# Performance work log

Measured on AMD Instinct MI355X. Metric: run time of the kernel, lower is better.

Reference implementation:

```python
import jax, jax.numpy as jnp
import numpy as np
import math

EMBED_DIM = 1024
NUM_HEADS = 16
HEAD_DIM = EMBED_DIM // NUM_HEADS


def setup_inputs() -> dict:
    key = jax.random.key(0)
    ks = jax.random.split(key, 5)
    s = 1.0 / math.sqrt(EMBED_DIM)
    return {
        "x": jax.random.normal(ks[0], (2, 2048, EMBED_DIM), dtype=jnp.float32),
        "w_qkv": jax.random.normal(ks[1], (EMBED_DIM, 3 * EMBED_DIM), dtype=jnp.float32) * s,
        "b_qkv": jax.random.normal(ks[2], (3 * EMBED_DIM,), dtype=jnp.float32) * 0.01,
        "w_proj": jax.random.normal(ks[3], (EMBED_DIM, EMBED_DIM), dtype=jnp.float32) * s,
        "b_proj": jax.random.normal(ks[4], (EMBED_DIM,), dtype=jnp.float32) * 0.01,
    }


def reference(x, w_qkv, b_qkv, w_proj, b_proj):
    B, T, C = x.shape
    qkv = (x @ w_qkv + b_qkv).reshape(B, T, 3, NUM_HEADS, HEAD_DIM)
    q, k, v = qkv[:, :, 0], qkv[:, :, 1], qkv[:, :, 2]  # [B,T,H,D]
    # scores: [B,H,T,T]
    att = jnp.einsum("bqhd,bkhd->bhqk", q, k) / math.sqrt(HEAD_DIM)
    causal = jnp.tril(jnp.ones((T, T), dtype=bool))
    att = jnp.where(causal[None, None], att, -jnp.inf)
    att = jax.nn.softmax(att, axis=-1)
    out = jnp.einsum("bhqk,bkhd->bqhd", att, v).reshape(B, T, C)
    return out @ w_proj + b_proj
```

## Files before the change

kernel.cpp:

```cpp
#include <hip/hip_runtime.h>
#include <stdint.h>


#define B_  2
#define T_  2048
#define C_  1024
#define NH  16
#define HD  64
#define BH_ (B_*NH)
#define M_  (B_*T_)

typedef __attribute__((ext_vector_type(8))) short short8;
typedef __attribute__((ext_vector_type(4))) float f32x4;
typedef __attribute__((ext_vector_type(4))) uint32_t u32x4;

typedef const __attribute__((address_space(1))) void* gas_ptr;
typedef __attribute__((address_space(3))) void* las_ptr;

__device__ __forceinline__ void gload_lds16(const void* g, void* l) {
  __builtin_amdgcn_global_load_lds((gas_ptr)g, (las_ptr)l, 16, 0, 0);
}

__device__ __forceinline__ unsigned short rne16(float x){
  uint32_t v = __float_as_uint(x);
  return (unsigned short)((v + 0x7fffu + ((v >> 16) & 1u)) >> 16);
}

__device__ __forceinline__ uint32_t cvtpk_bf16(float a, float b){
  uint32_t r;
  asm("v_cvt_pk_bf16_f32 %0, %1, %2" : "=v"(r) : "v"(a), "v"(b));
  return r;
}

__device__ __forceinline__ short8 hi8(u32x4 a, u32x4 b){
  union { u32x4 u; short8 s; } H;
  H.u[0] = __builtin_amdgcn_perm(a[1], a[0], 0x07060302u);
  H.u[1] = __builtin_amdgcn_perm(a[3], a[2], 0x07060302u);
  H.u[2] = __builtin_amdgcn_perm(b[1], b[0], 0x07060302u);
  H.u[3] = __builtin_amdgcn_perm(b[3], b[2], 0x07060302u);
  return H.s;
}
__device__ __forceinline__ short8 lo8(u32x4 a, u32x4 b){
  float l0 = __uint_as_float(a[0]) - __uint_as_float(a[0] & 0xffff0000u);
  float l1 = __uint_as_float(a[1]) - __uint_as_float(a[1] & 0xffff0000u);
  float l2 = __uint_as_float(a[2]) - __uint_as_float(a[2] & 0xffff0000u);
  float l3 = __uint_as_float(a[3]) - __uint_as_float(a[3] & 0xffff0000u);
  float l4 = __uint_as_float(b[0]) - __uint_as_float(b[0] & 0xffff0000u);
  float l5 = __uint_as_float(b[1]) - __uint_as_float(b[1] & 0xffff0000u);
  float l6 = __uint_as_float(b[2]) - __uint_as_float(b[2] & 0xffff0000u);
  float l7 = __uint_as_float(b[3]) - __uint_as_float(b[3] & 0xffff0000u);
  union { u32x4 u; short8 s; } L;
  L.u[0] = cvtpk_bf16(l0, l1);
  L.u[1] = cvtpk_bf16(l2, l3);
  L.u[2] = cvtpk_bf16(l4, l5);
  L.u[3] = cvtpk_bf16(l6, l7);
  return L.s;
}

__device__ __forceinline__ f32x4 mfma16(short8 a, short8 b, f32x4 c) {
  return __builtin_amdgcn_mfma_f32_16x16x32_bf16(a, b, c, 0, 0, 0);
}


__global__ __launch_bounds__(256) void pack4_kernel(const float4* __restrict__ in,
                                                    unsigned short* __restrict__ oh,
                                                    unsigned short* __restrict__ ol, int n4) {
  int i = blockIdx.x * 256 + threadIdx.x;
  if (i < n4) {
    float4 v = in[i];
    float f[4] = {v.x, v.y, v.z, v.w};
    ushort4 h, lo;
    unsigned short hh[4], ll[4];
    #pragma unroll
    for (int j=0;j<4;++j){
      uint32_t bt = __float_as_uint(f[j]);
      hh[j] = (unsigned short)(bt >> 16);
      ll[j] = rne16(f[j] - __uint_as_float(bt & 0xffff0000u));
    }
    h.x=hh[0]; h.y=hh[1]; h.z=hh[2]; h.w=hh[3];
    lo.x=ll[0]; lo.y=ll[1]; lo.z=ll[2]; lo.w=ll[3];
    *(ushort4*)(oh + (size_t)i*4) = h;
    *(ushort4*)(ol + (size_t)i*4) = lo;
  }
}

__global__ __launch_bounds__(1024) void pack_t_kernel(const float* __restrict__ in,
                                                      unsigned short* __restrict__ oh,
                                                      unsigned short* __restrict__ ol,
                                                      int R, int C) {
  __shared__ float tile[64][65];
  int c0 = blockIdx.x * 64, r0 = blockIdx.y * 64;
  int tx = threadIdx.x, ty = threadIdx.y;
  #pragma unroll
  for (int i = 0; i < 4; ++i)
    tile[ty + 16*i][tx] = in[(size_t)(r0 + ty + 16*i)*C + c0 + tx];
  __syncthreads();
  #pragma unroll
  for (int i = 0; i < 4; ++i) {
    float v = tile[tx][ty + 16*i];
    uint32_t bt = __float_as_uint(v);
    size_t o = (size_t)(c0 + ty + 16*i)*R + r0 + tx;
    oh[o] = (unsigned short)(bt >> 16);
    ol[o] = rne16(v - __uint_as_float(bt & 0xffff0000u));
  }
}


template<int MODE>
__global__ __launch_bounds__(256) void gemm_planes(
    const unsigned short* __restrict__ Ah, const unsigned short* __restrict__ Al,
    const unsigned short* __restrict__ Bh, const unsigned short* __restrict__ Bl,
    const float* __restrict__ bias,
    unsigned short* __restrict__ qh, unsigned short* __restrict__ ql,
    unsigned short* __restrict__ kh, unsigned short* __restrict__ kl,
    unsigned short* __restrict__ vth, unsigned short* __restrict__ vtl,
    float* __restrict__ fout, int M, int N, int K) {
  __shared__ unsigned short As[128*64];
  __shared__ unsigned short Bs[128*64];
  int tid = threadIdx.x;
  int w = tid >> 6, l = tid & 63, lg = l >> 4, lr = l & 15, lr7 = lr & 7;
  int bm = blockIdx.y * 128, bn = blockIdx.x * 128;
  int wm = (w >> 1) * 64, wn = (w & 1) * 64;

  const unsigned short* asrc[4]; const unsigned short* bsrc[4];
  #pragma unroll
  for (int i = 0; i < 4; ++i) {
    int s = tid + 256*i; int r = s >> 3, p = s & 7, u = p ^ (r & 7);
    asrc[i] = ((u < 4) ? Ah : Al) + (size_t)(bm + r)*K + (u & 3)*8;
    bsrc[i] = ((u < 4) ? Bh : Bl) + (size_t)(bn + r)*K + (u & 3)*8;
  }
  int aoh[4], boh[4];
  #pragma unroll
  for (int f = 0; f < 4; ++f) {
    aoh[f] = (wm + f*16 + lr)*128 + ((lg ^ lr7)*16);
    boh[f] = (wn + f*16 + lr)*128 + ((lg ^ lr7)*16);
  }

  f32x4 zero = {0.f, 0.f, 0.f, 0.f};
  f32x4 acc[4][4];
  #pragma unroll
  for (int i = 0; i < 4; ++i)
    #pragma unroll
    for (int j = 0; j < 4; ++j) acc[i][j] = zero;

  for (int k0 = 0; k0 < K; k0 += 32) {
    #pragma unroll
    for (int i = 0; i < 4; ++i) {
      int s = tid + 256*i;
      gload_lds16(asrc[i], (char*)As + (size_t)s*16);
      gload_lds16(bsrc[i], (char*)Bs + (size_t)s*16);
      asrc[i] += 32; bsrc[i] += 32;
    }
    __syncthreads();
    short8 ahf[4], alf[4];
    #pragma unroll
    for (int mf = 0; mf < 4; ++mf) {
      ahf[mf] = *(const short8*)((const char*)As + aoh[mf]);
      alf[mf] = *(const short8*)((const char*)As + (aoh[mf] ^ 64));
    }
    #pragma unroll
    for (int nf = 0; nf < 4; ++nf) {
      short8 bhf = *(const short8*)((const char*)Bs + boh[nf]);
      short8 blf = *(const short8*)((const char*)Bs + (boh[nf] ^ 64));
      #pragma unroll
      for (int mf = 0; mf < 4; ++mf) {
        acc[mf][nf] = mfma16(ahf[mf], bhf, acc[mf][nf]);
        acc[mf][nf] = mfma16(ahf[mf], blf, acc[mf][nf]);
        acc[mf][nf] = mfma16(alf[mf], bhf, acc[mf][nf]);
      }
    }
    __syncthreads();
  }
  #pragma unroll
  for (int nf = 0; nf < 4; ++nf) {
    int col = bn + wn + nf*16 + lr;
    float bv = bias[col];
    #pragma unroll
    for (int mf = 0; mf < 4; ++mf) {
      #pragma unroll
      for (int r = 0; r < 4; ++r) {
        int rowm = bm + wm + mf*16 + lg*4 + r;
        float v = acc[mf][nf][r] + bv;
        if (MODE == 1) {
          fout[(size_t)rowm*N + col] = v;
        } else {
          int sec = col >> 10;
          int hh  = (col >> 6) & 15;
          int d   = col & 63;
          int b   = rowm >> 11, t = rowm & 2047;
          size_t bhh = (size_t)b*NH + hh;
          if (sec == 0) v *= 0.125f;
          uint32_t bt = __float_as_uint(v);
          unsigned short h16 = (unsigned short)(bt >> 16);
          unsigned short l16 = rne16(v - __uint_as_float(bt & 0xffff0000u));
          if (sec == 0)      { size_t o = (bhh*T_ + t)*HD + d;  qh[o] = h16;  ql[o] = l16; }
          else if (sec == 1) { size_t o = (bhh*T_ + t)*HD + d;  kh[o] = h16;  kl[o] = l16; }
          else               { size_t o = (bhh*HD + d)*T_ + t;  vth[o] = h16; vtl[o] = l16; }
        }
      }
    }
  }
}


__global__ __launch_bounds__(256) void attn_kernel(
    const unsigned short* __restrict__ qh, const unsigned short* __restrict__ ql,
    const unsigned short* __restrict__ kh, const unsigned short* __restrict__ kl,
    const unsigned short* __restrict__ vth, const unsigned short* __restrict__ vtl,
    unsigned short* __restrict__ ctxh, unsigned short* __restrict__ ctxl) {
  __shared__ unsigned short Kt[2][64*128];
  __shared__ unsigned short Vt[2][64*128];
  __shared__ float Pf[4][1024];
  int bx = blockIdx.x;
  int xcd = bx & 7, jj = bx >> 3;
  int bh = xcd*4 + (jj >> 5);
  int qt = 31 - (jj & 31);
  int tid = threadIdx.x;
  int w = tid >> 6, l = tid & 63, lg = l >> 4, lr = l & 15, lr7 = lr & 7;
  int q0 = qt * 64;

  const unsigned short* qbh = qh + ((size_t)bh*T_ + q0 + w*16 + lr)*HD;
  const unsigned short* qbl = ql + ((size_t)bh*T_ + q0 + w*16 + lr)*HD;
  short8 qfh[2], qfl[2];
  #pragma unroll
  for (int ks = 0; ks < 2; ++ks) {
    qfh[ks] = *(const short8*)(qbh + ks*32 + lg*8);
    qfl[ks] = *(const short8*)(qbl + ks*32 + lg*8);
  }

  const unsigned short* ksrc[4]; const unsigned short* vsrc[4];
  #pragma unroll
  for (int i = 0; i < 4; ++i) {
    int s = tid + 256*i; int r = s >> 4, p = s & 15;
    int u = (p & 8) | ((p & 7) ^ (r & 7));
    ksrc[i] = ((u < 8) ? kh : kl) + ((size_t)bh*T_ + r)*HD + (u & 7)*8;
    vsrc[i] = ((u < 8) ? vth : vtl) + ((size_t)bh*HD + r)*T_ + (u & 7)*8;
  }
  auto stage = [&](int buf) {
    #pragma unroll
    for (int i = 0; i < 4; ++i) {
      int s = tid + 256*i;
      gload_lds16(ksrc[i], (char*)&Kt[buf][0] + (size_t)s*16);
      gload_lds16(vsrc[i], (char*)&Vt[buf][0] + (size_t)s*16);
    }
    #pragma unroll
    for (int i = 0; i < 4; ++i) { ksrc[i] += 64*HD; vsrc[i] += 64; }
  };

  int koff[4][2];
  #pragma unroll
  for (int fc = 0; fc < 4; ++fc)
    #pragma unroll
    for (int ks = 0; ks < 2; ++ks)
      koff[fc][ks] = (fc*16 + lr)*256 + (((ks*4 + lg) ^ lr7)*16);
  int pwoff[16];
  #pragma unroll
  for (int fc = 0; fc < 4; ++fc)
    #pragma unroll
    for (int r = 0; r < 4; ++r) {
      int q = lg*4 + r;
      int u = fc*4 + (lr >> 2);
      pwoff[fc*4 + r] = q*256 + ((u ^ q)*16) + (lr & 3)*4;
    }
  int proff[2][2];
  #pragma unroll
  for (int ks = 0; ks < 2; ++ks)
    #pragma unroll
    for (int g = 0; g < 2; ++g)
      proff[ks][g] = lr*256 + (((ks*8 + lg*2 + g) ^ lr)*16);

  f32x4 zero = {0.f, 0.f, 0.f, 0.f};
  f32x4 o[4] = {zero, zero, zero, zero};
  float m_r[4] = {-1e30f, -1e30f, -1e30f, -1e30f};
  float l_r[4] = {0.f, 0.f, 0.f, 0.f};
  char* PW = (char*)&Pf[w][0];

  stage(0);
  __syncthreads();
  int cur = 0;

  for (int kt = 0; kt <= qt; ++kt) {
    if (kt < qt) stage(cur ^ 1);
    const char* KB = (const char*)&Kt[cur][0];
    const char* VB = (const char*)&Vt[cur][0];
    f32x4 s4[4];
    #pragma unroll
    for (int fc = 0; fc < 4; ++fc) {
      f32x4 acc = zero;
      #pragma unroll
      for (int ks = 0; ks < 2; ++ks) {
        short8 khf = *(const short8*)(KB + koff[fc][ks]);
        short8 klf = *(const short8*)(KB + koff[fc][ks] + 128);
        acc = mfma16(qfh[ks], khf, acc);
        acc = mfma16(qfh[ks], klf, acc);
        acc = mfma16(qfl[ks], khf, acc);
      }
      s4[fc] = acc;
    }
    if (kt == qt) {
      #pragma unroll
      for (int fc = 0; fc < 4; ++fc)
        #pragma unroll
        for (int r = 0; r < 4; ++r) {
          int col = q0 + fc*16 + lr;
          int rw  = q0 + w*16 + lg*4 + r;
          if (col > rw) s4[fc][r] = -1e30f;
        }
    }
    float sc[4];
    #pragma unroll
    for (int r = 0; r < 4; ++r) {
      float v = fmaxf(fmaxf(s4[0][r], s4[1][r]), fmaxf(s4[2][r], s4[3][r]));
      v = fmaxf(v, __shfl_xor(v, 1));
      v = fmaxf(v, __shfl_xor(v, 2));
      v = fmaxf(v, __shfl_xor(v, 4));
      v = fmaxf(v, __shfl_xor(v, 8));
      float mn = fmaxf(m_r[r], v);
      sc[r] = __expf(m_r[r] - mn);
      m_r[r] = mn;
    }
    float sum[4] = {0.f, 0.f, 0.f, 0.f};
    #pragma unroll
    for (int fc = 0; fc < 4; ++fc)
      #pragma unroll
      for (int r = 0; r < 4; ++r) {
        float p = __expf(s4[fc][r] - m_r[r]);
        s4[fc][r] = p;
        sum[r] += p;
      }
    #pragma unroll
    for (int r = 0; r < 4; ++r) {
      float v = sum[r];
      v += __shfl_xor(v, 1); v += __shfl_xor(v, 2);
      v += __shfl_xor(v, 4); v += __shfl_xor(v, 8);
      l_r[r] = l_r[r]*sc[r] + v;
    }
    #pragma unroll
    for (int df = 0; df < 4; ++df)
      #pragma unroll
      for (int r = 0; r < 4; ++r) o[df][r] *= sc[r];
    #pragma unroll
    for (int fc = 0; fc < 4; ++fc)
      #pragma unroll
      for (int r = 0; r < 4; ++r)
        *(float*)(PW + pwoff[fc*4 + r]) = s4[fc][r];
    __builtin_amdgcn_sched_barrier(0);
    short8 pah[2], pal[2];
    #pragma unroll
    for (int ks = 0; ks < 2; ++ks) {
      u32x4 a = *(const u32x4*)(PW + proff[ks][0]);
      u32x4 b = *(const u32x4*)(PW + proff[ks][1]);
      pah[ks] = hi8(a, b);
      pal[ks] = lo8(a, b);
    }
    #pragma unroll
    for (int df = 0; df < 4; ++df) {
      #pragma unroll
      for (int ks = 0; ks < 2; ++ks) {
        short8 vhf = *(const short8*)(VB + koff[df][ks]);
        short8 vlf = *(const short8*)(VB + koff[df][ks] + 128);
        o[df] = mfma16(pah[ks], vhf, o[df]);
        o[df] = mfma16(pah[ks], vlf, o[df]);
        o[df] = mfma16(pal[ks], vhf, o[df]);
      }
    }
    __syncthreads();
    cur ^= 1;
  }
  int b = bh >> 4, h = bh & 15;
  float inv[4];
  #pragma unroll
  for (int r = 0; r < 4; ++r) inv[r] = 1.0f / l_r[r];
  #pragma unroll
  for (int df = 0; df < 4; ++df)
    #pragma unroll
    for (int r = 0; r < 4; ++r) {
      int q = q0 + w*16 + lg*4 + r;
      float v = o[df][r] * inv[r];
      uint32_t bt = __float_as_uint(v);
      size_t oo = ((size_t)b*T_ + q)*C_ + h*HD + df*16 + lr;
      ctxh[oo] = (unsigned short)(bt >> 16);
      ctxl[oo] = rne16(v - __uint_as_float(bt & 0xffff0000u));
    }
}


extern "C" void kernel_launch(void* const* d_in, const int* in_sizes, int n_in,
                              void* d_out, int out_size, void* d_ws, size_t ws_size,
                              hipStream_t stream) {
  (void)in_sizes; (void)n_in; (void)out_size; (void)ws_size;
  const float* x      = (const float*)d_in[0];
  const float* w_qkv  = (const float*)d_in[1];
  const float* b_qkv  = (const float*)d_in[2];
  const float* w_proj = (const float*)d_in[3];
  const float* b_proj = (const float*)d_in[4];
  float* out = (float*)d_out;

  uint8_t* ws = (uint8_t*)d_ws;
  const size_t MB = (size_t)1 << 20;
  unsigned short* xh  = (unsigned short*)(ws + 0);
  unsigned short* xl  = (unsigned short*)(ws + 8*MB);
  unsigned short* cth = xh;
  unsigned short* ctl = xl;
  unsigned short* wqh = (unsigned short*)(ws + 16*MB);
  unsigned short* wql = (unsigned short*)(ws + 22*MB);
  unsigned short* wph = (unsigned short*)(ws + 28*MB);
  unsigned short* wpl = (unsigned short*)(ws + 30*MB);
  unsigned short* qhp = (unsigned short*)(ws + 32*MB);
  unsigned short* qlp = (unsigned short*)(ws + 40*MB);
  unsigned short* khp = (unsigned short*)(ws + 48*MB);
  unsigned short* klp = (unsigned short*)(ws + 56*MB);
  unsigned short* vth = (unsigned short*)(ws + 64*MB);
  unsigned short* vtl = (unsigned short*)(ws + 72*MB);

  pack4_kernel<<<(M_*C_/4 + 255)/256, 256, 0, stream>>>((const float4*)x, xh, xl, M_*C_/4);
  pack_t_kernel<<<dim3(3*C_/64, C_/64), dim3(64, 16), 0, stream>>>(w_qkv, wqh, wql, C_, 3*C_);
  pack_t_kernel<<<dim3(C_/64, C_/64), dim3(64, 16), 0, stream>>>(w_proj, wph, wpl, C_, C_);
  gemm_planes<0><<<dim3(3*C_/128, M_/128), 256, 0, stream>>>(
      xh, xl, wqh, wql, b_qkv, qhp, qlp, khp, klp, vth, vtl, nullptr, M_, 3*C_, C_);
  attn_kernel<<<dim3(1024), 256, 0, stream>>>(qhp, qlp, khp, klp, vth, vtl, cth, ctl);
  gemm_planes<1><<<dim3(C_/128, M_/128), 256, 0, stream>>>(
      cth, ctl, wph, wpl, b_proj, nullptr, nullptr, nullptr, nullptr, nullptr, nullptr,
      out, M_, C_, C_);
}
```

Baseline: 384.1 us.

## Restructure attention: transposed S, register P shuffle, 32-key tiles, lazy rescale

Rewrites the flash-attention loop to compute S transposed (K as the A operand) so each lane owns one query row. P now reaches the PV MFMA through cross-lane shuffles instead of an LDS round trip, which removes the Pf buffer. KV tiles shrink to 32 keys, and per-wave causal skipping drops tiles a wave does not need. A lazy max-rescale only rescales when the new max exceeds the old one by more than 8. It also reorders blocks for load balance, sets a 4-block occupancy bound and vectorises the output stores. The cost is twice as many barriers per key range and extra shuffle work per tile.

```diff
diff --git a/kernel.cpp b/kernel.cpp
--- a/kernel.cpp
+++ b/kernel.cpp
@@ -30,31 +30,6 @@
   uint32_t r;
   asm("v_cvt_pk_bf16_f32 %0, %1, %2" : "=v"(r) : "v"(a), "v"(b));
   return r;
-}
-
-__device__ __forceinline__ short8 hi8(u32x4 a, u32x4 b){
-  union { u32x4 u; short8 s; } H;
-  H.u[0] = __builtin_amdgcn_perm(a[1], a[0], 0x07060302u);
-  H.u[1] = __builtin_amdgcn_perm(a[3], a[2], 0x07060302u);
-  H.u[2] = __builtin_amdgcn_perm(b[1], b[0], 0x07060302u);
-  H.u[3] = __builtin_amdgcn_perm(b[3], b[2], 0x07060302u);
-  return H.s;
-}
-__device__ __forceinline__ short8 lo8(u32x4 a, u32x4 b){
-  float l0 = __uint_as_float(a[0]) - __uint_as_float(a[0] & 0xffff0000u);
-  float l1 = __uint_as_float(a[1]) - __uint_as_float(a[1] & 0xffff0000u);
-  float l2 = __uint_as_float(a[2]) - __uint_as_float(a[2] & 0xffff0000u);
-  float l3 = __uint_as_float(a[3]) - __uint_as_float(a[3] & 0xffff0000u);
-  float l4 = __uint_as_float(b[0]) - __uint_as_float(b[0] & 0xffff0000u);
-  float l5 = __uint_as_float(b[1]) - __uint_as_float(b[1] & 0xffff0000u);
-  float l6 = __uint_as_float(b[2]) - __uint_as_float(b[2] & 0xffff0000u);
-  float l7 = __uint_as_float(b[3]) - __uint_as_float(b[3] & 0xffff0000u);
-  union { u32x4 u; short8 s; } L;
-  L.u[0] = cvtpk_bf16(l0, l1);
-  L.u[1] = cvtpk_bf16(l2, l3);
-  L.u[2] = cvtpk_bf16(l4, l5);
-  L.u[3] = cvtpk_bf16(l6, l7);
-  return L.s;
 }
 
 __device__ __forceinline__ f32x4 mfma16(short8 a, short8 b, f32x4 c) {
@@ -203,24 +178,25 @@
 }
 
 
-__global__ __launch_bounds__(256) void attn_kernel(
+__global__ __launch_bounds__(256, 4) void attn_kernel(
     const unsigned short* __restrict__ qh, const unsigned short* __restrict__ ql,
     const unsigned short* __restrict__ kh, const unsigned short* __restrict__ kl,
     const unsigned short* __restrict__ vth, const unsigned short* __restrict__ vtl,
     unsigned short* __restrict__ ctxh, unsigned short* __restrict__ ctxl) {
-  __shared__ unsigned short Kt[2][64*128];
-  __shared__ unsigned short Vt[2][64*128];
-  __shared__ float Pf[4][1024];
-  int bx = blockIdx.x;
-  int xcd = bx & 7, jj = bx >> 3;
-  int bh = xcd*4 + (jj >> 5);
-  int qt = 31 - (jj & 31);
+  __shared__ unsigned short Kt[2][32*128];
+  __shared__ unsigned short Vt[2][64*64];
+  int b = blockIdx.x;
+  int xcd = b & 7, bh_lo = (b >> 3) & 3, jj = (b >> 5) & 7, kk = b >> 8;
+  int bh = xcd*4 + bh_lo;
+  int qt = (kk == 0) ? jj : (kk == 1) ? 15 - jj : (kk == 2) ? 16 + jj : 31 - jj;
+  int q0 = qt * 64;
   int tid = threadIdx.x;
-  int w = tid >> 6, l = tid & 63, lg = l >> 4, lr = l & 15, lr7 = lr & 7;
-  int q0 = qt * 64;
-
-  const unsigned short* qbh = qh + ((size_t)bh*T_ + q0 + w*16 + lr)*HD;
-  const unsigned short* qbl = ql + ((size_t)bh*T_ + q0 + w*16 + lr)*HD;
+  int w = tid >> 6, l = tid & 63, lg = l >> 4, lr = l & 15;
+  int q0w = q0 + w*16;
+  int qrow = q0w + lr;
+
+  const unsigned short* qbh = qh + ((size_t)bh*T_ + qrow)*HD;
+  const unsigned short* qbl = ql + ((size_t)bh*T_ + qrow)*HD;
   short8 qfh[2], qfl[2];
   #pragma unroll
   for (int ks = 0; ks < 2; ++ks) {
@@ -228,160 +204,168 @@
     qfl[ks] = *(const short8*)(qbl + ks*32 + lg*8);
   }
 
-  const unsigned short* ksrc[4]; const unsigned short* vsrc[4];
-  #pragma unroll
-  for (int i = 0; i < 4; ++i) {
-    int s = tid + 256*i; int r = s >> 4, p = s & 15;
-    int u = (p & 8) | ((p & 7) ^ (r & 7));
-    ksrc[i] = ((u < 8) ? kh : kl) + ((size_t)bh*T_ + r)*HD + (u & 7)*8;
-    vsrc[i] = ((u < 8) ? vth : vtl) + ((size_t)bh*HD + r)*T_ + (u & 7)*8;
+  const unsigned short* ksrc[2]; const unsigned short* vsrc[2];
+  #pragma unroll
+  for (int i = 0; i < 2; ++i) {
+    int s = tid + 256*i;
+    { int r = s >> 4, p = s & 15, u = (p & 8) | ((p & 7) ^ (r & 7));
+      ksrc[i] = ((u < 8) ? kh : kl) + ((size_t)bh*T_ + r)*HD + (u & 7)*8; }
+    { int r = s >> 3, p = s & 7, u = p ^ (r & 7);
+      vsrc[i] = ((u < 4) ? vth : vtl) + ((size_t)bh*HD + r)*T_ + (u & 3)*8; }
   }
   auto stage = [&](int buf) {
     #pragma unroll
-    for (int i = 0; i < 4; ++i) {
+    for (int i = 0; i < 2; ++i) {
       int s = tid + 256*i;
       gload_lds16(ksrc[i], (char*)&Kt[buf][0] + (size_t)s*16);
       gload_lds16(vsrc[i], (char*)&Vt[buf][0] + (size_t)s*16);
-    }
-    #pragma unroll
-    for (int i = 0; i < 4; ++i) { ksrc[i] += 64*HD; vsrc[i] += 64; }
+      ksrc[i] += 32*HD;
+      vsrc[i] += 32;
+    }
   };
 
-  int koff[4][2];
-  #pragma unroll
-  for (int fc = 0; fc < 4; ++fc)
-    #pragma unroll
-    for (int ks = 0; ks < 2; ++ks)
-      koff[fc][ks] = (fc*16 + lr)*256 + (((ks*4 + lg) ^ lr7)*16);
-  int pwoff[16];
-  #pragma unroll
-  for (int fc = 0; fc < 4; ++fc)
-    #pragma unroll
-    for (int r = 0; r < 4; ++r) {
-      int q = lg*4 + r;
-      int u = fc*4 + (lr >> 2);
-      pwoff[fc*4 + r] = q*256 + ((u ^ q)*16) + (lr & 3)*4;
-    }
-  int proff[2][2];
-  #pragma unroll
-  for (int ks = 0; ks < 2; ++ks)
-    #pragma unroll
-    for (int g = 0; g < 2; ++g)
-      proff[ks][g] = lr*256 + (((ks*8 + lg*2 + g) ^ lr)*16);
+  int koff[2][2];
+  #pragma unroll
+  for (int fc = 0; fc < 2; ++fc)
+    #pragma unroll
+    for (int ks = 0; ks < 2; ++ks) {
+      int row = fc*16 + lr;
+      koff[fc][ks] = row*256 + (((ks*4 + lg) ^ (row & 7))*16);
+    }
+  int voff[4];
+  #pragma unroll
+  for (int df = 0; df < 4; ++df) {
+    int row = df*16 + lr;
+    voff[df] = row*128 + ((lg ^ (row & 7))*16);
+  }
 
   f32x4 zero = {0.f, 0.f, 0.f, 0.f};
   f32x4 o[4] = {zero, zero, zero, zero};
-  float m_r[4] = {-1e30f, -1e30f, -1e30f, -1e30f};
-  float l_r[4] = {0.f, 0.f, 0.f, 0.f};
-  char* PW = (char*)&Pf[w][0];
-
+  float m_r = -1e30f, l_r = 0.f;
+
+  int nkt = 2*qt + 2;
   stage(0);
   __syncthreads();
   int cur = 0;
 
-  for (int kt = 0; kt <= qt; ++kt) {
-    if (kt < qt) stage(cur ^ 1);
-    const char* KB = (const char*)&Kt[cur][0];
-    const char* VB = (const char*)&Vt[cur][0];
-    f32x4 s4[4];
-    #pragma unroll
-    for (int fc = 0; fc < 4; ++fc) {
-      f32x4 acc = zero;
-      #pragma unroll
-      for (int ks = 0; ks < 2; ++ks) {
-        short8 khf = *(const short8*)(KB + koff[fc][ks]);
-        short8 klf = *(const short8*)(KB + koff[fc][ks] + 128);
-        acc = mfma16(qfh[ks], khf, acc);
-        acc = mfma16(qfh[ks], klf, acc);
-        acc = mfma16(qfl[ks], khf, acc);
-      }
-      s4[fc] = acc;
-    }
-    if (kt == qt) {
-      #pragma unroll
-      for (int fc = 0; fc < 4; ++fc)
+  int sl = lr + ((lg & 1) << 5);
+  int sh = sl + 16;
+  bool lglo = lg < 2;
+
+  for (int kt = 0; kt < nkt; ++kt) {
+    int kv0 = kt*32;
+    if (kt + 1 < nkt) stage(cur ^ 1);
+    if (kv0 <= q0w + 15) {
+      const char* KB = (const char*)&Kt[cur][0];
+      const char* VB = (const char*)&Vt[cur][0];
+      f32x4 st[2];
+      #pragma unroll
+      for (int fc = 0; fc < 2; ++fc) {
+        f32x4 acc = zero;
+        #pragma unroll
+        for (int ks = 0; ks < 2; ++ks) {
+          short8 khf = *(const short8*)(KB + koff[fc][ks]);
+          short8 klf = *(const short8*)(KB + koff[fc][ks] + 128);
+          acc = mfma16(khf, qfh[ks], acc);
+          acc = mfma16(khf, qfl[ks], acc);
+          acc = mfma16(klf, qfh[ks], acc);
+        }
+        st[fc] = acc;
+      }
+      if (kv0 + 31 > q0w) {
+        #pragma unroll
+        for (int fc = 0; fc < 2; ++fc)
+          #pragma unroll
+          for (int r = 0; r < 4; ++r) {
+            int kv = kv0 + fc*16 + lg*4 + r;
+            if (kv > qrow) st[fc][r] = -1e30f;
+          }
+      }
+      float pm = fmaxf(fmaxf(fmaxf(st[0][0], st[0][1]), fmaxf(st[0][2], st[0][3])),
+                       fmaxf(fmaxf(st[1][0], st[1][1]), fmaxf(st[1][2], st[1][3])));
+      pm = fmaxf(pm, __shfl_xor(pm, 16));
+      pm = fmaxf(pm, __shfl_xor(pm, 32));
+      if (__any(pm > m_r + 8.f)) {
+        float mn = fmaxf(m_r, pm);
+        float sc = __expf(m_r - mn);
+        m_r = mn; l_r *= sc;
+        #pragma unroll
+        for (int df = 0; df < 4; ++df)
+          #pragma unroll
+          for (int r = 0; r < 4; ++r) o[df][r] *= sc;
+      }
+      float sum = 0.f;
+      #pragma unroll
+      for (int fc = 0; fc < 2; ++fc)
         #pragma unroll
         for (int r = 0; r < 4; ++r) {
-          int col = q0 + fc*16 + lr;
-          int rw  = q0 + w*16 + lg*4 + r;
-          if (col > rw) s4[fc][r] = -1e30f;
+          float p = __expf(st[fc][r] - m_r);
+          st[fc][r] = p;
+          sum += p;
         }
-    }
-    float sc[4];
-    #pragma unroll
-    for (int r = 0; r < 4; ++r) {
-      float v = fmaxf(fmaxf(s4[0][r], s4[1][r]), fmaxf(s4[2][r], s4[3][r]));
-      v = fmaxf(v, __shfl_xor(v, 1));
-      v = fmaxf(v, __shfl_xor(v, 2));
-      v = fmaxf(v, __shfl_xor(v, 4));
-      v = fmaxf(v, __shfl_xor(v, 8));
-      float mn = fmaxf(m_r[r], v);
-      sc[r] = __expf(m_r[r] - mn);
-      m_r[r] = mn;
-    }
-    float sum[4] = {0.f, 0.f, 0.f, 0.f};
-    #pragma unroll
-    for (int fc = 0; fc < 4; ++fc)
-      #pragma unroll
-      for (int r = 0; r < 4; ++r) {
-        float p = __expf(s4[fc][r] - m_r[r]);
-        s4[fc][r] = p;
-        sum[r] += p;
-      }
-    #pragma unroll
-    for (int r = 0; r < 4; ++r) {
-      float v = sum[r];
-      v += __shfl_xor(v, 1); v += __shfl_xor(v, 2);
-      v += __shfl_xor(v, 4); v += __shfl_xor(v, 8);
-      l_r[r] = l_r[r]*sc[r] + v;
-    }
-    #pragma unroll
-    for (int df = 0; df < 4; ++df)
-      #pragma unroll
-      for (int r = 0; r < 4; ++r) o[df][r] *= sc[r];
-    #pragma unroll
-    for (int fc = 0; fc < 4; ++fc)
-      #pragma unroll
-      for (int r = 0; r < 4; ++r)
-        *(float*)(PW + pwoff[fc*4 + r]) = s4[fc][r];
-    __builtin_amdgcn_sched_barrier(0);
-    short8 pah[2], pal[2];
-    #pragma unroll
-    for (int ks = 0; ks < 2; ++ks) {
-      u32x4 a = *(const u32x4*)(PW + proff[ks][0]);
-      u32x4 b = *(const u32x4*)(PW + proff[ks][1]);
-      pah[ks] = hi8(a, b);
-      pal[ks] = lo8(a, b);
-    }
-    #pragma unroll
-    for (int df = 0; df < 4; ++df) {
-      #pragma unroll
-      for (int ks = 0; ks < 2; ++ks) {
-        short8 vhf = *(const short8*)(VB + koff[df][ks]);
-        short8 vlf = *(const short8*)(VB + koff[df][ks] + 128);
-        o[df] = mfma16(pah[ks], vhf, o[df]);
-        o[df] = mfma16(pah[ks], vlf, o[df]);
-        o[df] = mfma16(pal[ks], vhf, o[df]);
+      sum += __shfl_xor(sum, 16);
+      sum += __shfl_xor(sum, 32);
+      l_r += sum;
+      uint32_t Hpk[2][2], Lpk[2][2];
+      #pragma unroll
+      for (int fc = 0; fc < 2; ++fc)
+        #pragma unroll
+        for (int i = 0; i < 2; ++i) {
+          float pe = st[fc][2*i], po = st[fc][2*i + 1];
+          uint32_t H = cvtpk_bf16(pe, po);
+          Hpk[fc][i] = H;
+          float fe = __uint_as_float(H << 16);
+          float fo = __uint_as_float(H & 0xffff0000u);
+          Lpk[fc][i] = cvtpk_bf16(pe - fe, po - fo);
+        }
+      union { u32x4 u; short8 s; } BH, BL;
+      {
+        int a0 = __shfl((int)Hpk[0][0], sl), b0 = __shfl((int)Hpk[1][0], sl);
+        int a1 = __shfl((int)Hpk[0][1], sl), b1 = __shfl((int)Hpk[1][1], sl);
+        int a2 = __shfl((int)Hpk[0][0], sh), b2 = __shfl((int)Hpk[1][0], sh);
+        int a3 = __shfl((int)Hpk[0][1], sh), b3 = __shfl((int)Hpk[1][1], sh);
+        BH.u[0] = lglo ? a0 : b0; BH.u[1] = lglo ? a1 : b1;
+        BH.u[2] = lglo ? a2 : b2; BH.u[3] = lglo ? a3 : b3;
+      }
+      {
+        int a0 = __shfl((int)Lpk[0][0], sl), b0 = __shfl((int)Lpk[1][0], sl);
+        int a1 = __shfl((int)Lpk[0][1], sl), b1 = __shfl((int)Lpk[1][1], sl);
+        int a2 = __shfl((int)Lpk[0][0], sh), b2 = __shfl((int)Lpk[1][0], sh);
+        int a3 = __shfl((int)Lpk[0][1], sh), b3 = __shfl((int)Lpk[1][1], sh);
+        BL.u[0] = lglo ? a0 : b0; BL.u[1] = lglo ? a1 : b1;
+        BL.u[2] = lglo ? a2 : b2; BL.u[3] = lglo ? a3 : b3;
+      }
+      #pragma unroll
+      for (int df = 0; df < 4; ++df) {
+        short8 vhf = *(const short8*)(VB + voff[df]);
+        short8 vlf = *(const short8*)(VB + (voff[df] ^ 64));
+        o[df] = mfma16(vhf, BH.s, o[df]);
+        o[df] = mfma16(vhf, BL.s, o[df]);
+        o[df] = mfma16(vlf, BH.s, o[df]);
       }
     }
     __syncthreads();
     cur ^= 1;
   }
-  int b = bh >> 4, h = bh & 15;
-  float inv[4];
-  #pragma unroll
-  for (int r = 0; r < 4; ++r) inv[r] = 1.0f / l_r[r];
-  #pragma unroll
-  for (int df = 0; df < 4; ++df)
+  int bb = bh >> 4, h = bh & 15;
+  float inv = 1.0f / l_r;
+  #pragma unroll
+  for (int df = 0; df < 4; ++df) {
+    ushort4 hv, lv;
+    unsigned short hh[4], ll[4];
     #pragma unroll
     for (int r = 0; r < 4; ++r) {
-      int q = q0 + w*16 + lg*4 + r;
-      float v = o[df][r] * inv[r];
+      float v = o[df][r] * inv;
       uint32_t bt = __float_as_uint(v);
-      size_t oo = ((size_t)b*T_ + q)*C_ + h*HD + df*16 + lr;
-      ctxh[oo] = (unsigned short)(bt >> 16);
-      ctxl[oo] = rne16(v - __uint_as_float(bt & 0xffff0000u));
-    }
+      hh[r] = (unsigned short)(bt >> 16);
+      ll[r] = rne16(v - __uint_as_float(bt & 0xffff0000u));
+    }
+    hv.x=hh[0]; hv.y=hh[1]; hv.z=hh[2]; hv.w=hh[3];
+    lv.x=ll[0]; lv.y=ll[1]; lv.z=ll[2]; lv.w=ll[3];
+    size_t oo = ((size_t)bb*T_ + qrow)*C_ + h*HD + df*16 + lg*4;
+    *(ushort4*)&ctxh[oo] = hv;
+    *(ushort4*)&ctxl[oo] = lv;
+  }
 }
 
 
```

Result: faster. 355.2 us (-7.5%).
